# Kernel tuning notes

Measured on AMD Instinct MI355X. Metric: run time of the kernel, lower is better.

## Reference

```python
import jax, jax.numpy as jnp
import numpy as np

N = 100000
E = 3200000
H = 32
L = 2
LN_EPS = 1e-5


def _layer_norm(x, g, b):
    mu = jnp.mean(x, axis=-1, keepdims=True)
    var = jnp.mean(jnp.square(x - mu), axis=-1, keepdims=True)
    return (x - mu) * jax.lax.rsqrt(var + LN_EPS) * g + b


def setup_inputs() -> dict:
    key = jax.random.key(0)
    ks = jax.random.split(key, 32)
    aa_idx = jax.random.randint(ks[0], (N,), 0, 21)
    atom_idx = jax.random.randint(ks[1], (N,), 0, 3)
    edge_index = jax.random.randint(ks[2], (2, E), 0, N)
    edge_attr = jax.random.uniform(ks[3], (E, 4), dtype=jnp.float32)
    edge_attr = edge_attr.at[:, 0].multiply(30.0)  # distances in [0, 30)
    s = 0.1
    p = {
        'aa_emb': jax.random.normal(ks[4], (21, 16), jnp.float32) * s,
        'atom_emb': jax.random.normal(ks[5], (3, 16), jnp.float32) * s,
        'proj_W1': jax.random.normal(ks[6], (32, H), jnp.float32) * s,
        'proj_b1': jnp.zeros((H,), jnp.float32),
        'proj_W2': jax.random.normal(ks[7], (H, H), jnp.float32) * s,
        'proj_b2': jnp.zeros((H,), jnp.float32),
        'short_eps': jnp.zeros((L,), jnp.float32),
        'short_eW': jax.random.normal(ks[8], (L, 4, H), jnp.float32) * s,
        'short_eb': jnp.zeros((L, H), jnp.float32),
        'short_W1': jax.random.normal(ks[9], (L, H, H), jnp.float32) * s,
        'short_b1': jnp.zeros((L, H), jnp.float32),
        'short_W2': jax.random.normal(ks[10], (L, H, H), jnp.float32) * s,
        'short_b2': jnp.zeros((L, H), jnp.float32),
        'long_eps': jnp.zeros((L,), jnp.float32),
        'long_eW': jax.random.normal(ks[11], (L, 4, H), jnp.float32) * s,
        'long_eb': jnp.zeros((L, H), jnp.float32),
        'long_W1': jax.random.normal(ks[12], (L, H, H), jnp.float32) * s,
        'long_b1': jnp.zeros((L, H), jnp.float32),
        'long_W2': jax.random.normal(ks[13], (L, H, H), jnp.float32) * s,
        'long_b2': jnp.zeros((L, H), jnp.float32),
        'ln_g': jnp.ones((L, H), jnp.float32),
        'ln_b': jnp.zeros((L, H), jnp.float32),
        'head_W1': jax.random.normal(ks[14], (H, 16), jnp.float32) * s,
        'head_b1': jnp.zeros((16,), jnp.float32),
        'head_W2': jax.random.normal(ks[15], (16, 8), jnp.float32) * s,
        'head_b2': jnp.zeros((8,), jnp.float32),
        'head_W3': jax.random.normal(ks[16], (8, 8), jnp.float32) * s,
        'head_b3': jnp.zeros((8,), jnp.float32),
    }
    return dict(aa_idx=aa_idx, atom_idx=atom_idx, edge_index=edge_index, edge_attr=edge_attr, **p)


def _gine(h, edge_attr, src, dst, mask, eps, eW, eb, W1, b1, W2, b2):
    # GINEConv: msg = relu(x_src + lin(edge_attr)); sum into dst; nn((1+eps)*x + aggr)
    msg = jax.nn.relu(h[src] + edge_attr @ eW + eb) * mask[:, None]
    aggr = jax.ops.segment_sum(msg, dst, num_segments=h.shape[0])
    z = (1.0 + eps) * h + aggr
    return jax.nn.relu(z @ W1 + b1) @ W2 + b2


def reference(aa_idx, atom_idx, edge_index, edge_attr,
              aa_emb, atom_emb, proj_W1, proj_b1, proj_W2, proj_b2,
              short_eps, short_eW, short_eb, short_W1, short_b1, short_W2, short_b2,
              long_eps, long_eW, long_eb, long_W1, long_b1, long_W2, long_b2,
              ln_g, ln_b, head_W1, head_b1, head_W2, head_b2, head_W3, head_b3):
    x = jnp.concatenate([aa_emb[aa_idx], atom_emb[atom_idx]], axis=-1)  # [N, 32]
    h = jax.nn.relu(x @ proj_W1 + proj_b1) @ proj_W2 + proj_b2  # [N, H]

    dist = edge_attr[:, 0]
    src, dst = edge_index[0], edge_index[1]
    ca = (atom_idx == 1)
    short_mask = ((dist >= 0.0) & (dist < 10.0)).astype(h.dtype)
    long_mask = ((dist >= 0.0) & (dist <= 25.0) & ca[src] & ca[dst]).astype(h.dtype)

    for l in range(L):
        h_s = _gine(h, edge_attr, src, dst, short_mask, short_eps[l], short_eW[l], short_eb[l], short_W1[l], short_b1[l], short_W2[l], short_b2[l])
        h_l = _gine(h, edge_attr, src, dst, long_mask, long_eps[l], long_eW[l], long_eb[l], long_W1[l], long_b1[l], long_W2[l], long_b2[l])
        h = _layer_norm(h + h_s + h_l, ln_g[l], ln_b[l])
        h = jax.nn.relu(h)  # dropout is identity in eval mode

    h = jax.nn.relu(h @ head_W1 + head_b1)
    h = jax.nn.relu(h @ head_W2 + head_b2)
    return h @ head_W3 + head_b3  # [N, 8]
```

## Files before the change

### kernel.cpp

```cpp
#include <hip/hip_runtime.h>

#define NN 100000
#define NE 3200000
#define CAP 1500000
#define NBUCK 391
#define BK_CAP 4096
#define PP_EPT 4
#define PP_BS 1024
#define NBLK ((NE + PP_BS * PP_EPT - 1) / (PP_BS * PP_EPT))

typedef unsigned long long u64;
typedef unsigned int u32;


__device__ __forceinline__ void mv32(const float* __restrict__ W,
                                     const float* __restrict__ b,
                                     const float* __restrict__ x,
                                     float* __restrict__ o, bool do_relu) {
#pragma unroll
  for (int c = 0; c < 32; ++c) o[c] = b[c];
#pragma unroll
  for (int k = 0; k < 32; ++k) {
    float xk = x[k];
#pragma unroll
    for (int c = 0; c < 32; ++c) o[c] = fmaf(xk, W[k * 32 + c], o[c]);
  }
  if (do_relu) {
#pragma unroll
    for (int c = 0; c < 32; ++c) o[c] = fmaxf(o[c], 0.f);
  }
}

__global__ __launch_bounds__(256) void k_init(
    const int* __restrict__ aa_idx, const int* __restrict__ atom_idx,
    const float* __restrict__ aa_emb, const float* __restrict__ atom_emb,
    const float* __restrict__ W1, const float* __restrict__ b1,
    const float* __restrict__ W2, const float* __restrict__ b2,
    float* __restrict__ h) {
  __shared__ float sW1[1024], sW2[1024], sb1[32], sb2[32];
  int t = threadIdx.x;
  for (int i = t; i < 1024; i += 256) { sW1[i] = W1[i]; sW2[i] = W2[i]; }
  if (t < 32) { sb1[t] = b1[t]; sb2[t] = b2[t]; }
  __syncthreads();
  int n = blockIdx.x * 256 + t;
  if (n >= NN) return;
  int aa = aa_idx[n], at = atom_idx[n];
  float x[32];
  const float4* ar = (const float4*)(aa_emb + aa * 16);
  const float4* trp = (const float4*)(atom_emb + at * 16);
#pragma unroll
  for (int q = 0; q < 4; ++q) {
    float4 v = ar[q];
    x[q*4+0]=v.x; x[q*4+1]=v.y; x[q*4+2]=v.z; x[q*4+3]=v.w;
  }
#pragma unroll
  for (int q = 0; q < 4; ++q) {
    float4 v = trp[q];
    x[16+q*4+0]=v.x; x[16+q*4+1]=v.y; x[16+q*4+2]=v.z; x[16+q*4+3]=v.w;
  }
  float tmp[32], o[32];
  mv32(sW1, sb1, x, tmp, true);
  mv32(sW2, sb2, tmp, o, false);
  float4* hrow = (float4*)(h + (size_t)n * 32);
#pragma unroll
  for (int q = 0; q < 8; ++q)
    hrow[q] = make_float4(o[q*4], o[q*4+1], o[q*4+2], o[q*4+3]);
}

__global__ __launch_bounds__(PP_BS) void k_preprocess(
    const int* __restrict__ edge_index, const float4* __restrict__ edge_attr,
    const int* __restrict__ atom_idx,
    uint4* __restrict__ elist, int* __restrict__ cnt,
    int* __restrict__ hist, int* __restrict__ segStart, int* __restrict__ segCnt) {
  __shared__ int swc[PP_BS / 64];
  __shared__ int sbase;
  __shared__ int lhist[NBUCK];
  int t = threadIdx.x;
  for (int i = t; i < NBUCK; i += PP_BS) lhist[i] = 0;
  __syncthreads();
  int lane = t & 63, wid = t >> 6;
  int base = blockIdx.x * (PP_BS * PP_EPT) + t;
  uint4 ent[PP_EPT];
  unsigned mbs[PP_EPT];
  int pre[PP_EPT];
  int wtot = 0;
#pragma unroll
  for (int q = 0; q < PP_EPT; ++q) {
    int e = base + q * PP_BS;
    unsigned mb = 0;
    uint4 en = make_uint4(0, 0, 0, 0);
    if (e < NE) {
      float4 a = edge_attr[e];
      float dist = a.x;
      if (dist >= 0.f && dist <= 25.f) {
        int s = edge_index[e];
        int d = edge_index[NE + e];
        unsigned sb = (dist < 10.f) ? 1u : 0u;
        unsigned lb = (atom_idx[s] == 1 && atom_idx[d] == 1) ? 2u : 0u;
        mb = sb | lb;
        if (mb) {
          u32 cat = (mb == 1u) ? 0u : ((mb == 3u) ? 1u : 2u);
          u32 qx = (u32)(dist * (65535.f / 25.f) + 0.5f);
          u32 qy = (u32)(a.y * 65535.f + 0.5f);
          u32 qz = (u32)(a.z * 65535.f + 0.5f);
          u32 qw = (u32)(a.w * 65535.f + 0.5f);
          en.x = (u32)s | (cat << 17);
          en.y = (u32)d;
          en.z = qx | (qy << 16);
          en.w = qz | (qw << 16);
          atomicAdd(&lhist[d >> 8], 1);
        }
      }
    }
    ent[q] = en; mbs[q] = mb;
    unsigned long long bal = __ballot(mb != 0);
    pre[q] = wtot + __popcll(bal & ((1ull << lane) - 1ull));
    wtot += (int)__popcll(bal);
  }
  if (lane == 0) swc[wid] = wtot;
  __syncthreads();
  if (t == 0) {
    int tot = 0;
#pragma unroll
    for (int w = 0; w < PP_BS / 64; ++w) { int c = swc[w]; swc[w] = tot; tot += c; }
    sbase = atomicAdd(cnt, tot);
    segStart[blockIdx.x] = sbase;
    segCnt[blockIdx.x] = tot;
  }
  __syncthreads();
  int mybase = sbase + swc[wid];
#pragma unroll
  for (int q = 0; q < PP_EPT; ++q)
    if (mbs[q]) elist[mybase + pre[q]] = ent[q];
  for (int i = t; i < NBUCK; i += PP_BS)
    hist[(size_t)blockIdx.x * NBUCK + i] = lhist[i];
}

__global__ __launch_bounds__(1024) void kA(
    const int* __restrict__ hist, int* __restrict__ cpT, int* __restrict__ bucketTotal) {
  __shared__ int s[1024];
  int b = blockIdx.x;
  int t = threadIdx.x;
  int v = (t < NBLK) ? hist[(size_t)t * NBUCK + b] : 0;
  s[t] = v;
  __syncthreads();
  for (int off = 1; off < 1024; off <<= 1) {
    int a = (t >= off) ? s[t - off] : 0;
    __syncthreads();
    s[t] += a;
    __syncthreads();
  }
  if (t < NBLK) cpT[(size_t)t * NBUCK + b] = s[t] - v;
  if (t == NBLK - 1) bucketTotal[b] = s[t];
}

__global__ __launch_bounds__(512) void kB(
    const int* __restrict__ bucketTotal, int* __restrict__ bucketBase,
    int* __restrict__ row_ptr) {
  __shared__ int sc[512];
  int t = threadIdx.x;
  int v0 = (t < NBUCK) ? bucketTotal[t] : 0;
  sc[t] = v0;
  __syncthreads();
  for (int off = 1; off < 512; off <<= 1) {
    int a = (t >= off) ? sc[t - off] : 0;
    __syncthreads();
    sc[t] += a;
    __syncthreads();
  }
  int incl = sc[t];
  if (t < NBUCK) bucketBase[t] = incl - v0;
  if (t == NBUCK - 1) { bucketBase[NBUCK] = incl; row_ptr[NN] = incl; }
}

__global__ __launch_bounds__(256) void k_place(
    const uint4* __restrict__ elist, const int* __restrict__ segStart,
    const int* __restrict__ segCnt, const int* __restrict__ bucketBase,
    const int* __restrict__ cpT, uint4* __restrict__ part) {
  __shared__ int baseB[NBUCK];
  __shared__ int cur[NBUCK];
  int k = blockIdx.x;
  int t = threadIdx.x;
  for (int b = t; b < NBUCK; b += 256) {
    baseB[b] = bucketBase[b] + cpT[(size_t)k * NBUCK + b];
    cur[b] = 0;
  }
  __syncthreads();
  int s0 = segStart[k], n0 = segCnt[k];
  for (int i = t; i < n0; i += 256) {
    uint4 en = elist[s0 + i];
    int b = (int)(en.y >> 8);
    int r = atomicAdd(&cur[b], 1);
    part[baseB[b] + r] = en;
  }
}

__global__ __launch_bounds__(1024) void k_sort(
    const uint4* __restrict__ part, const int* __restrict__ bucketBase,
    uint4* __restrict__ rec, int* __restrict__ row_ptr, u32* __restrict__ m12) {
  __shared__ uint4 sbuf[BK_CAP];
  __shared__ int hist[768], cur[768];
  __shared__ int wpart[4];
  int b = blockIdx.x;
  int t = threadIdx.x;
  int base = bucketBase[b];
  int cntB = bucketBase[b + 1] - base;
  if (cntB > BK_CAP) cntB = BK_CAP;
  if (t < 768) hist[t] = 0;
  __syncthreads();
  for (int i = t; i < cntB; i += 1024) {
    uint4 en = part[base + i];
    sbuf[i] = en;
    int bin = (int)(en.y & 255u) * 3 + (int)(en.x >> 17);
    atomicAdd(&hist[bin], 1);
  }
  __syncthreads();
  int h0 = 0, h1 = 0, s0 = 0, inc = 0;
  int lane = t & 63;
  if (t < 256) {
    h0 = hist[3 * t]; h1 = hist[3 * t + 1];
    int h2 = hist[3 * t + 2];
    s0 = h0 + h1 + h2;
    inc = s0;
#pragma unroll
    for (int d = 1; d < 64; d <<= 1) {
      int o = __shfl_up(inc, d);
      if (lane >= d) inc += o;
    }
    if (lane == 63) wpart[t >> 6] = inc;
  }
  __syncthreads();
  if (t < 256) {
    int woff = 0;
#pragma unroll
    for (int w = 0; w < 4; ++w)
      if (w < (t >> 6)) woff += wpart[w];
    int ex = woff + inc - s0;
    cur[3 * t] = ex; cur[3 * t + 1] = ex + h0; cur[3 * t + 2] = ex + h0 + h1;
    int node = b * 256 + t;
    if (node < NN) {
      row_ptr[node] = base + ex;
      m12[node] = (u32)h0 | ((u32)(h0 + h1) << 16);
    }
  }
  __syncthreads();
  for (int i = t; i < cntB; i += 1024) {
    uint4 en = sbuf[i];
    int bin = (int)(en.y & 255u) * 3 + (int)(en.x >> 17);
    int r = atomicAdd(&cur[bin], 1);
    rec[base + r] = en;
  }
}

#define AG_BLOCKS 4096
__device__ __forceinline__ float edge_msg(
    uint4 r, int c, const float* __restrict__ h,
    float w0, float w1, float w2, float w3, float bb) {
  int s = (int)(r.x & 0x1FFFFu);
  float hv = h[(size_t)s * 32 + c];
  float ax = (float)(r.z & 0xFFFFu);
  float ay = (float)(r.z >> 16);
  float az = (float)(r.w & 0xFFFFu);
  float aw = (float)(r.w >> 16);
  float tt = bb + ax * w0 + ay * w1 + az * w2 + aw * w3;
  return fmaxf(hv + tt, 0.f);
}

__global__ __launch_bounds__(256) void k_aggr(
    const int* __restrict__ row_ptr, const u32* __restrict__ m12,
    const uint4* __restrict__ rec, const float* __restrict__ h,
    float* __restrict__ aggr_s, float* __restrict__ aggr_l,
    const float* __restrict__ eW_s, const float* __restrict__ eb_s,
    const float* __restrict__ eW_l, const float* __restrict__ eb_l) {
  int t = threadIdx.x;
  int lane = t & 63;
  int c = lane & 31;
  int half = lane >> 5;
  int wave = (blockIdx.x * 256 + t) >> 6;
  int nwaves = (gridDim.x * 256) >> 6;
  const float qd = 25.f / 65535.f, q1 = 1.f / 65535.f;
  float ws0 = eW_s[c] * qd, ws1 = eW_s[32 + c] * q1,
        ws2 = eW_s[64 + c] * q1, ws3 = eW_s[96 + c] * q1;
  float bs = eb_s[c];
  float wl0 = eW_l[c] * qd, wl1 = eW_l[32 + c] * q1,
        wl2 = eW_l[64 + c] * q1, wl3 = eW_l[96 + c] * q1;
  float bl = eb_l[c];
  for (int node = wave; node < NN; node += nwaves) {
    int start = row_ptr[node];
    int end = row_ptr[node + 1];
    u32 mm = m12[node];
    int m1 = start + (int)(mm & 0xFFFFu);
    int m2 = start + (int)(mm >> 16);
    float acc_s = 0.f;
    int i = start + half;
    for (; i + 2 < m2; i += 4) {
      uint4 r0 = rec[i];
      uint4 r1 = rec[i + 2];
      acc_s += edge_msg(r0, c, h, ws0, ws1, ws2, ws3, bs);
      acc_s += edge_msg(r1, c, h, ws0, ws1, ws2, ws3, bs);
    }
    if (i < m2) acc_s += edge_msg(rec[i], c, h, ws0, ws1, ws2, ws3, bs);
    float acc_l = 0.f;
    i = m1 + half;
    for (; i + 2 < end; i += 4) {
      uint4 r0 = rec[i];
      uint4 r1 = rec[i + 2];
      acc_l += edge_msg(r0, c, h, wl0, wl1, wl2, wl3, bl);
      acc_l += edge_msg(r1, c, h, wl0, wl1, wl2, wl3, bl);
    }
    if (i < end) acc_l += edge_msg(rec[i], c, h, wl0, wl1, wl2, wl3, bl);
    float rs = acc_s + __shfl_xor(acc_s, 32);
    float rl = acc_l + __shfl_xor(acc_l, 32);
    if (half == 0) aggr_s[(size_t)node * 32 + c] = rs;
    else           aggr_l[(size_t)node * 32 + c] = rl;
  }
}

template <bool LAST>
__global__ __launch_bounds__(256) void k_node(
    float* __restrict__ h, const float* __restrict__ aggr_s, const float* __restrict__ aggr_l,
    const float* __restrict__ eps_s, const float* __restrict__ eps_l,
    const float* __restrict__ W1s, const float* __restrict__ b1s,
    const float* __restrict__ W2s, const float* __restrict__ b2s,
    const float* __restrict__ W1l, const float* __restrict__ b1l,
    const float* __restrict__ W2l, const float* __restrict__ b2l,
    const float* __restrict__ lng, const float* __restrict__ lnb,
    const float* __restrict__ hW1, const float* __restrict__ hb1,
    const float* __restrict__ hW2, const float* __restrict__ hb2,
    const float* __restrict__ hW3, const float* __restrict__ hb3,
    float* __restrict__ out) {
  __shared__ float sW1s[1024], sW2s[1024], sW1l[1024], sW2l[1024];
  __shared__ float sb1s[32], sb2s[32], sb1l[32], sb2l[32], sg[32], sbn[32];
  __shared__ float sh1[512], sh2[128], sh3[64], shb1[16], shb2[8], shb3[8];
  int t = threadIdx.x;
  for (int i = t; i < 1024; i += 256) {
    sW1s[i] = W1s[i]; sW2s[i] = W2s[i]; sW1l[i] = W1l[i]; sW2l[i] = W2l[i];
  }
  if (t < 32) {
    sb1s[t] = b1s[t]; sb2s[t] = b2s[t]; sb1l[t] = b1l[t]; sb2l[t] = b2l[t];
    sg[t] = lng[t]; sbn[t] = lnb[t];
  }
  if (LAST) {
    for (int i = t; i < 512; i += 256) sh1[i] = hW1[i];
    if (t < 128) sh2[t] = hW2[t];
    if (t < 64) sh3[t] = hW3[t];
    if (t < 16) shb1[t] = hb1[t];
    if (t < 8) { shb2[t] = hb2[t]; shb3[t] = hb3[t]; }
  }
  __syncthreads();
  float es = 1.f + eps_s[0];
  float el = 1.f + eps_l[0];
  int n = blockIdx.x * 256 + t;
  if (n >= NN) return;
  float4* hrow = (float4*)(h + (size_t)n * 32);
  const float4* asr = (const float4*)(aggr_s + (size_t)n * 32);
  const float4* alr = (const float4*)(aggr_l + (size_t)n * 32);
  float hv[32], x[32], z[32], tt[32];
#pragma unroll
  for (int q = 0; q < 8; ++q) {
    float4 v = hrow[q];
    hv[q*4+0]=v.x; hv[q*4+1]=v.y; hv[q*4+2]=v.z; hv[q*4+3]=v.w;
  }
#pragma unroll
  for (int q = 0; q < 8; ++q) {
    float4 v = asr[q];
    z[q*4+0]=v.x; z[q*4+1]=v.y; z[q*4+2]=v.z; z[q*4+3]=v.w;
  }
#pragma unroll
  for (int c = 0; c < 32; ++c) z[c] = fmaf(es, hv[c], z[c]);
  mv32(sW1s, sb1s, z, tt, true);
  mv32(sW2s, sb2s, tt, x, false);
#pragma unroll
  for (int c = 0; c < 32; ++c) x[c] += hv[c];
#pragma unroll
  for (int q = 0; q < 8; ++q) {
    float4 v = alr[q];
    z[q*4+0]=v.x; z[q*4+1]=v.y; z[q*4+2]=v.z; z[q*4+3]=v.w;
  }
#pragma unroll
  for (int c = 0; c < 32; ++c) z[c] = fmaf(el, hv[c], z[c]);
  mv32(sW1l, sb1l, z, tt, true);
  mv32(sW2l, sb2l, tt, hv, false);
#pragma unroll
  for (int c = 0; c < 32; ++c) x[c] += hv[c];
  float mu = 0.f;
#pragma unroll
  for (int c = 0; c < 32; ++c) mu += x[c];
  mu *= (1.f / 32.f);
  float var = 0.f;
#pragma unroll
  for (int c = 0; c < 32; ++c) { float dd = x[c] - mu; var += dd * dd; }
  var *= (1.f / 32.f);
  float rs = rsqrtf(var + 1e-5f);
#pragma unroll
  for (int c = 0; c < 32; ++c) {
    float y = (x[c] - mu) * rs * sg[c] + sbn[c];
    x[c] = fmaxf(y, 0.f);
  }
  if (!LAST) {
#pragma unroll
    for (int q = 0; q < 8; ++q)
      hrow[q] = make_float4(x[q*4], x[q*4+1], x[q*4+2], x[q*4+3]);
  } else {
    float t16[16];
#pragma unroll
    for (int j = 0; j < 16; ++j) t16[j] = shb1[j];
#pragma unroll
    for (int k = 0; k < 32; ++k) {
      float xk = x[k];
#pragma unroll
      for (int j = 0; j < 16; ++j) t16[j] = fmaf(xk, sh1[k * 16 + j], t16[j]);
    }
#pragma unroll
    for (int j = 0; j < 16; ++j) t16[j] = fmaxf(t16[j], 0.f);
    float t8[8];
#pragma unroll
    for (int j = 0; j < 8; ++j) t8[j] = shb2[j];
#pragma unroll
    for (int k = 0; k < 16; ++k) {
      float xk = t16[k];
#pragma unroll
      for (int j = 0; j < 8; ++j) t8[j] = fmaf(xk, sh2[k * 8 + j], t8[j]);
    }
#pragma unroll
    for (int j = 0; j < 8; ++j) t8[j] = fmaxf(t8[j], 0.f);
    float o8[8];
#pragma unroll
    for (int j = 0; j < 8; ++j) o8[j] = shb3[j];
#pragma unroll
    for (int k = 0; k < 8; ++k) {
      float xk = t8[k];
#pragma unroll
      for (int j = 0; j < 8; ++j) o8[j] = fmaf(xk, sh3[k * 8 + j], o8[j]);
    }
    float4* orow = (float4*)(out + (size_t)n * 8);
    orow[0] = make_float4(o8[0], o8[1], o8[2], o8[3]);
    orow[1] = make_float4(o8[4], o8[5], o8[6], o8[7]);
  }
}

extern "C" void kernel_launch(void* const* d_in, const int* in_sizes, int n_in,
                              void* d_out, int out_size, void* d_ws, size_t ws_size,
                              hipStream_t stream) {
  const int*   aa_idx     = (const int*)d_in[0];
  const int*   atom_idx   = (const int*)d_in[1];
  const int*   edge_index = (const int*)d_in[2];
  const float* edge_attr  = (const float*)d_in[3];
  const float* aa_emb     = (const float*)d_in[4];
  const float* atom_emb   = (const float*)d_in[5];
  const float* proj_W1    = (const float*)d_in[6];
  const float* proj_b1    = (const float*)d_in[7];
  const float* proj_W2    = (const float*)d_in[8];
  const float* proj_b2    = (const float*)d_in[9];
  const float* short_eps  = (const float*)d_in[10];
  const float* short_eW   = (const float*)d_in[11];
  const float* short_eb   = (const float*)d_in[12];
  const float* short_W1   = (const float*)d_in[13];
  const float* short_b1   = (const float*)d_in[14];
  const float* short_W2   = (const float*)d_in[15];
  const float* short_b2   = (const float*)d_in[16];
  const float* long_eps   = (const float*)d_in[17];
  const float* long_eW    = (const float*)d_in[18];
  const float* long_eb    = (const float*)d_in[19];
  const float* long_W1    = (const float*)d_in[20];
  const float* long_b1    = (const float*)d_in[21];
  const float* long_W2    = (const float*)d_in[22];
  const float* long_b2    = (const float*)d_in[23];
  const float* ln_g       = (const float*)d_in[24];
  const float* ln_b       = (const float*)d_in[25];
  const float* head_W1    = (const float*)d_in[26];
  const float* head_b1    = (const float*)d_in[27];
  const float* head_W2    = (const float*)d_in[28];
  const float* head_b2    = (const float*)d_in[29];
  const float* head_W3    = (const float*)d_in[30];
  const float* head_b3    = (const float*)d_in[31];
  float* out = (float*)d_out;

  char* p = (char*)d_ws;
  uint4* rec     = (uint4*)p;                 p += (size_t)CAP * 16;
  uint4* elist   = (uint4*)p;                 p += (size_t)CAP * 16;
  float* h       = (float*)p;                 p += (size_t)NN * 32 * 4;
  float* aggr_s  = (float*)p;                 p += (size_t)NN * 32 * 4;
  float* aggr_l  = (float*)p;                 p += (size_t)NN * 32 * 4;
  int*   row_ptr = (int*)p;                   p += (size_t)(NN + 1) * 4;
  u32*   m12     = (u32*)p;                   p += (size_t)NN * 4;
  int*   hist    = (int*)p;                   p += (size_t)NBLK * NBUCK * 4;
  int*   cpT     = (int*)p;                   p += (size_t)NBLK * NBUCK * 4;
  int*   segStart= (int*)p;                   p += (size_t)NBLK * 4;
  int*   segCnt  = (int*)p;                   p += (size_t)NBLK * 4;
  int*   bucketBase = (int*)p;                p += (size_t)(NBUCK + 1) * 4;
  int*   bucketTotal= (int*)p;                p += (size_t)NBUCK * 4;
  int*   cnt     = (int*)p;
  uint4* part    = (uint4*)aggr_s;

  hipMemsetAsync(cnt, 0, sizeof(int), stream);

  k_init<<<(NN + 255) / 256, 256, 0, stream>>>(
      aa_idx, atom_idx, aa_emb, atom_emb, proj_W1, proj_b1, proj_W2, proj_b2, h);

  k_preprocess<<<NBLK, PP_BS, 0, stream>>>(
      edge_index, (const float4*)edge_attr, atom_idx, elist, cnt,
      hist, segStart, segCnt);

  kA<<<NBUCK, 1024, 0, stream>>>(hist, cpT, bucketTotal);
  kB<<<1, 512, 0, stream>>>(bucketTotal, bucketBase, row_ptr);

  k_place<<<NBLK, 256, 0, stream>>>(
      elist, segStart, segCnt, bucketBase, cpT, part);

  k_sort<<<NBUCK, 1024, 0, stream>>>(part, bucketBase, rec, row_ptr, m12);

  for (int l = 0; l < 2; ++l) {
    k_aggr<<<AG_BLOCKS, 256, 0, stream>>>(
        row_ptr, m12, rec, h, aggr_s, aggr_l,
        short_eW + l * 128, short_eb + l * 32, long_eW + l * 128, long_eb + l * 32);
    if (l == 0) {
      k_node<false><<<(NN + 255) / 256, 256, 0, stream>>>(
          h, aggr_s, aggr_l, short_eps + l, long_eps + l,
          short_W1 + l * 1024, short_b1 + l * 32, short_W2 + l * 1024, short_b2 + l * 32,
          long_W1 + l * 1024, long_b1 + l * 32, long_W2 + l * 1024, long_b2 + l * 32,
          ln_g + l * 32, ln_b + l * 32,
          nullptr, nullptr, nullptr, nullptr, nullptr, nullptr, out);
    } else {
      k_node<true><<<(NN + 255) / 256, 256, 0, stream>>>(
          h, aggr_s, aggr_l, short_eps + l, long_eps + l,
          short_W1 + l * 1024, short_b1 + l * 32, short_W2 + l * 1024, short_b2 + l * 32,
          long_W1 + l * 1024, long_b1 + l * 32, long_W2 + l * 1024, long_b2 + l * 32,
          ln_g + l * 32, ln_b + l * 32,
          head_W1, head_b1, head_W2, head_b2, head_W3, head_b3, out);
    }
  }
}
```

Measured before the change: 297.3 us.

## Use shared-memory CA bitmask in preprocess and single-pass masked edge aggregation

Adds a kernel that packs the atom_idx==1 test into a 32-bit-per-word bitmask, which each preprocess block copies into shared memory. This replaces two random global loads of atom_idx per edge with shared lookups. The aggregation kernel now walks each node's edges in one pass and uses per-edge category masks to accumulate both the short and long sums, instead of two separate range loops driven by m12 offsets. That removes the m12 array and the re-read of overlapping edges. In exchange it adds a tiny extra kernel and computes both edge transforms for every edge.

Result: faster. 277.7 us (-6.6%).

```diff
diff --git a/kernel.cpp b/kernel.cpp
--- a/kernel.cpp
+++ b/kernel.cpp
@@ -8,6 +8,7 @@
 #define PP_EPT 4
 #define PP_BS 1024
 #define NBLK ((NE + PP_BS * PP_EPT - 1) / (PP_BS * PP_EPT))
+#define NW ((NN + 31) / 32)
 
 typedef unsigned long long u64;
 typedef unsigned int u32;
@@ -29,6 +30,18 @@
 #pragma unroll
     for (int c = 0; c < 32; ++c) o[c] = fmaxf(o[c], 0.f);
   }
+}
+
+__global__ __launch_bounds__(256) void k_ca(
+    const int* __restrict__ atom_idx, u32* __restrict__ caBits) {
+  int w = blockIdx.x * 256 + threadIdx.x;
+  if (w >= NW) return;
+  int base = w * 32;
+  int lim = NN - base; if (lim > 32) lim = 32;
+  u32 bits = 0;
+  for (int j = 0; j < lim; ++j)
+    bits |= (atom_idx[base + j] == 1 ? 1u : 0u) << j;
+  caBits[w] = bits;
 }
 
 __global__ __launch_bounds__(256) void k_init(
@@ -69,14 +82,16 @@
 
 __global__ __launch_bounds__(PP_BS) void k_preprocess(
     const int* __restrict__ edge_index, const float4* __restrict__ edge_attr,
-    const int* __restrict__ atom_idx,
+    const u32* __restrict__ caBits,
     uint4* __restrict__ elist, int* __restrict__ cnt,
     int* __restrict__ hist, int* __restrict__ segStart, int* __restrict__ segCnt) {
   __shared__ int swc[PP_BS / 64];
   __shared__ int sbase;
   __shared__ int lhist[NBUCK];
+  __shared__ u32 lcab[NW];
   int t = threadIdx.x;
   for (int i = t; i < NBUCK; i += PP_BS) lhist[i] = 0;
+  for (int i = t; i < NW; i += PP_BS) lcab[i] = caBits[i];
   __syncthreads();
   int lane = t & 63, wid = t >> 6;
   int base = blockIdx.x * (PP_BS * PP_EPT) + t;
@@ -96,7 +111,9 @@
         int s = edge_index[e];
         int d = edge_index[NE + e];
         unsigned sb = (dist < 10.f) ? 1u : 0u;
-        unsigned lb = (atom_idx[s] == 1 && atom_idx[d] == 1) ? 2u : 0u;
+        u32 cs = (lcab[(u32)s >> 5] >> (s & 31)) & 1u;
+        u32 cd = (lcab[(u32)d >> 5] >> (d & 31)) & 1u;
+        unsigned lb = (cs & cd) << 1;
         mb = sb | lb;
         if (mb) {
           u32 cat = (mb == 1u) ? 0u : ((mb == 3u) ? 1u : 2u);
@@ -197,7 +214,7 @@
 
 __global__ __launch_bounds__(1024) void k_sort(
     const uint4* __restrict__ part, const int* __restrict__ bucketBase,
-    uint4* __restrict__ rec, int* __restrict__ row_ptr, u32* __restrict__ m12) {
+    uint4* __restrict__ rec, int* __restrict__ row_ptr) {
   __shared__ uint4 sbuf[BK_CAP];
   __shared__ int hist[768], cur[768];
   __shared__ int wpart[4];
@@ -238,10 +255,7 @@
     int ex = woff + inc - s0;
     cur[3 * t] = ex; cur[3 * t + 1] = ex + h0; cur[3 * t + 2] = ex + h0 + h1;
     int node = b * 256 + t;
-    if (node < NN) {
-      row_ptr[node] = base + ex;
-      m12[node] = (u32)h0 | ((u32)(h0 + h1) << 16);
-    }
+    if (node < NN) row_ptr[node] = base + ex;
   }
   __syncthreads();
   for (int i = t; i < cntB; i += 1024) {
@@ -253,22 +267,29 @@
 }
 
 #define AG_BLOCKS 4096
-__device__ __forceinline__ float edge_msg(
+__device__ __forceinline__ void accum_edge(
     uint4 r, int c, const float* __restrict__ h,
-    float w0, float w1, float w2, float w3, float bb) {
+    float ws0, float ws1, float ws2, float ws3, float bs,
+    float wl0, float wl1, float wl2, float wl3, float bl,
+    float& acc_s, float& acc_l) {
   int s = (int)(r.x & 0x1FFFFu);
+  u32 cat = r.x >> 17;
   float hv = h[(size_t)s * 32 + c];
   float ax = (float)(r.z & 0xFFFFu);
   float ay = (float)(r.z >> 16);
   float az = (float)(r.w & 0xFFFFu);
   float aw = (float)(r.w >> 16);
-  float tt = bb + ax * w0 + ay * w1 + az * w2 + aw * w3;
-  return fmaxf(hv + tt, 0.f);
+  float ts = bs + ax * ws0 + ay * ws1 + az * ws2 + aw * ws3;
+  float tl = bl + ax * wl0 + ay * wl1 + az * wl2 + aw * wl3;
+  float ms = (cat <= 1u) ? 1.f : 0.f;
+  float ml = (cat >= 1u) ? 1.f : 0.f;
+  acc_s = fmaf(ms, fmaxf(hv + ts, 0.f), acc_s);
+  acc_l = fmaf(ml, fmaxf(hv + tl, 0.f), acc_l);
 }
 
 __global__ __launch_bounds__(256) void k_aggr(
-    const int* __restrict__ row_ptr, const u32* __restrict__ m12,
-    const uint4* __restrict__ rec, const float* __restrict__ h,
+    const int* __restrict__ row_ptr, const uint4* __restrict__ rec,
+    const float* __restrict__ h,
     float* __restrict__ aggr_s, float* __restrict__ aggr_l,
     const float* __restrict__ eW_s, const float* __restrict__ eb_s,
     const float* __restrict__ eW_l, const float* __restrict__ eb_l) {
@@ -288,27 +309,18 @@
   for (int node = wave; node < NN; node += nwaves) {
     int start = row_ptr[node];
     int end = row_ptr[node + 1];
-    u32 mm = m12[node];
-    int m1 = start + (int)(mm & 0xFFFFu);
-    int m2 = start + (int)(mm >> 16);
-    float acc_s = 0.f;
+    float acc_s = 0.f, acc_l = 0.f;
     int i = start + half;
-    for (; i + 2 < m2; i += 4) {
-      uint4 r0 = rec[i];
-      uint4 r1 = rec[i + 2];
-      acc_s += edge_msg(r0, c, h, ws0, ws1, ws2, ws3, bs);
-      acc_s += edge_msg(r1, c, h, ws0, ws1, ws2, ws3, bs);
-    }
-    if (i < m2) acc_s += edge_msg(rec[i], c, h, ws0, ws1, ws2, ws3, bs);
-    float acc_l = 0.f;
-    i = m1 + half;
     for (; i + 2 < end; i += 4) {
       uint4 r0 = rec[i];
       uint4 r1 = rec[i + 2];
-      acc_l += edge_msg(r0, c, h, wl0, wl1, wl2, wl3, bl);
-      acc_l += edge_msg(r1, c, h, wl0, wl1, wl2, wl3, bl);
-    }
-    if (i < end) acc_l += edge_msg(rec[i], c, h, wl0, wl1, wl2, wl3, bl);
+      accum_edge(r0, c, h, ws0, ws1, ws2, ws3, bs, wl0, wl1, wl2, wl3, bl, acc_s, acc_l);
+      accum_edge(r1, c, h, ws0, ws1, ws2, ws3, bs, wl0, wl1, wl2, wl3, bl, acc_s, acc_l);
+    }
+    if (i < end) {
+      uint4 r0 = rec[i];
+      accum_edge(r0, c, h, ws0, ws1, ws2, ws3, bs, wl0, wl1, wl2, wl3, bl, acc_s, acc_l);
+    }
     float rs = acc_s + __shfl_xor(acc_s, 32);
     float rl = acc_l + __shfl_xor(acc_l, 32);
     if (half == 0) aggr_s[(size_t)node * 32 + c] = rs;
@@ -483,23 +495,25 @@
   float* aggr_s  = (float*)p;                 p += (size_t)NN * 32 * 4;
   float* aggr_l  = (float*)p;                 p += (size_t)NN * 32 * 4;
   int*   row_ptr = (int*)p;                   p += (size_t)(NN + 1) * 4;
-  u32*   m12     = (u32*)p;                   p += (size_t)NN * 4;
   int*   hist    = (int*)p;                   p += (size_t)NBLK * NBUCK * 4;
   int*   cpT     = (int*)p;                   p += (size_t)NBLK * NBUCK * 4;
   int*   segStart= (int*)p;                   p += (size_t)NBLK * 4;
   int*   segCnt  = (int*)p;                   p += (size_t)NBLK * 4;
   int*   bucketBase = (int*)p;                p += (size_t)(NBUCK + 1) * 4;
   int*   bucketTotal= (int*)p;                p += (size_t)NBUCK * 4;
+  u32*   caBits  = (u32*)p;                   p += (size_t)NW * 4;
   int*   cnt     = (int*)p;
   uint4* part    = (uint4*)aggr_s;
 
   hipMemsetAsync(cnt, 0, sizeof(int), stream);
 
+  k_ca<<<(NW + 255) / 256, 256, 0, stream>>>(atom_idx, caBits);
+
   k_init<<<(NN + 255) / 256, 256, 0, stream>>>(
       aa_idx, atom_idx, aa_emb, atom_emb, proj_W1, proj_b1, proj_W2, proj_b2, h);
 
   k_preprocess<<<NBLK, PP_BS, 0, stream>>>(
-      edge_index, (const float4*)edge_attr, atom_idx, elist, cnt,
+      edge_index, (const float4*)edge_attr, caBits, elist, cnt,
       hist, segStart, segCnt);
 
   kA<<<NBUCK, 1024, 0, stream>>>(hist, cpT, bucketTotal);
@@ -508,11 +522,11 @@
   k_place<<<NBLK, 256, 0, stream>>>(
       elist, segStart, segCnt, bucketBase, cpT, part);
 
-  k_sort<<<NBUCK, 1024, 0, stream>>>(part, bucketBase, rec, row_ptr, m12);
+  k_sort<<<NBUCK, 1024, 0, stream>>>(part, bucketBase, rec, row_ptr);
 
   for (int l = 0; l < 2; ++l) {
     k_aggr<<<AG_BLOCKS, 256, 0, stream>>>(
-        row_ptr, m12, rec, h, aggr_s, aggr_l,
+        row_ptr, rec, h, aggr_s, aggr_l,
         short_eW + l * 128, short_eb + l * 32, long_eW + l * 128, long_eb + l * 32);
     if (l == 0) {
       k_node<false><<<(NN + 255) / 256, 256, 0, stream>>>(
```
